# Optimization experiments

Hardware: AMD Instinct MI355X
Metric: run time of the kernel (lower is better)

The kernel has to match this reference:

```python
import jax, jax.numpy as jnp
import numpy as np

D = 1024
H = 16
DH = D // H  # 64
EPS = 1e-6


def setup_inputs() -> dict:
    key = jax.random.key(0)
    ks = jax.random.split(key, 8)
    N, NQ, NK = 8, 1024, 1024
    queries = jax.random.normal(ks[0], (N, NQ, D), dtype=jnp.float32)
    keys = jax.random.normal(ks[1], (N, NK, D), dtype=jnp.float32)
    values = jax.random.normal(ks[2], (N, NK, D), dtype=jnp.float32)
    mask = jax.random.uniform(ks[3], (H * N, NQ, NK), dtype=jnp.float32)
    s = 1.0 / np.sqrt(D)
    Wq = jax.random.normal(ks[4], (H, DH, D), dtype=jnp.float32) * s  # per-head Linear(d, d_head) weights
    Wk = jax.random.normal(ks[5], (H, DH, D), dtype=jnp.float32) * s
    Wv = jax.random.normal(ks[6], (H, DH, D), dtype=jnp.float32) * s
    Wo = jax.random.normal(ks[7], (D, D), dtype=jnp.float32) * s
    return {"queries": queries, "keys": keys, "values": values, "mask": mask,
            "Wq": Wq, "Wk": Wk, "Wv": Wv, "Wo": Wo}


def reference(queries, keys, values, mask, Wq, Wk, Wv, Wo):
    N, NQ, _ = queries.shape
    NK = keys.shape[1]
    # per-head projections, fused into one batched einsum (head-major like torch.cat(dim=0))
    q = jnp.einsum('nqd,hed->hnqe', queries, Wq)  # [H, N, NQ, DH]
    k = jnp.einsum('nkd,hed->hnke', keys, Wk)
    v = jnp.einsum('nkd,hed->hnke', values, Wv)
    scores = jnp.einsum('hnqe,hnke->hnqk', q, k) / jnp.sqrt(jnp.float32(DH))
    att = jax.nn.softmax(scores, axis=-1)  # [H, N, NQ, NK]
    m = mask.reshape(H, N, NQ, NK)
    att = att * m
    att = att / (att.sum(axis=-1, keepdims=True) + EPS)
    o = jnp.einsum('hnqk,hnke->hnqe', att, v)  # [H, N, NQ, DH]
    # concat heads along feature dim: [N, NQ, H*DH]
    o = o.transpose(1, 2, 0, 3).reshape(N, NQ, D)
    return o @ Wo.T
```

## Files before the change

### kernel.cpp

```cpp
#include <hip/hip_runtime.h>
#include <stdint.h>

#define DEV static __device__ __forceinline__

typedef __attribute__((ext_vector_type(8))) short shortx8;
typedef __attribute__((ext_vector_type(4))) float floatx4;
typedef __attribute__((ext_vector_type(4))) unsigned short ushortx4;
typedef __attribute__((ext_vector_type(4))) unsigned int uintx4;


DEV unsigned short f2bf(float x) {
  unsigned int u = __float_as_uint(x);
  u += 0x7fffu + ((u >> 16) & 1u);
  return (unsigned short)(u >> 16);
}

DEV unsigned int cvtpk(float lo, float hi) {
  unsigned int r;
  asm("v_cvt_pk_bf16_f32 %0, %1, %2" : "=v"(r) : "v"(lo), "v"(hi));
  return r;
}

DEV void async16(const void* g, void* l) {
  __builtin_amdgcn_global_load_lds(
      (const __attribute__((address_space(1))) void*)g,
      (__attribute__((address_space(3))) void*)l, 16, 0, 0);
}

__global__ __launch_bounds__(256) void cast_all(
    const float* __restrict__ xq, const float* __restrict__ xk, const float* __restrict__ xv,
    const float* __restrict__ wq, const float* __restrict__ wk, const float* __restrict__ wv,
    const float* __restrict__ wo,
    unsigned short* __restrict__ oxq, unsigned short* __restrict__ oxk, unsigned short* __restrict__ oxv,
    unsigned short* __restrict__ owq, unsigned short* __restrict__ owk, unsigned short* __restrict__ owv,
    unsigned short* __restrict__ owo) {
  int b = blockIdx.x;
  const float* in;
  unsigned short* out;
  size_t i;
  if (b < 12288) {
    int which = b >> 12;
    in = which == 0 ? xq : (which == 1 ? xk : xv);
    out = which == 0 ? oxq : (which == 1 ? oxk : oxv);
    i = (size_t)(b & 4095) * 256 + threadIdx.x;
  } else {
    int bb = b - 12288;
    int which = bb >> 9;
    in = which == 0 ? wq : (which == 1 ? wk : (which == 2 ? wv : wo));
    out = which == 0 ? owq : (which == 1 ? owk : (which == 2 ? owv : owo));
    i = (size_t)(bb & 511) * 256 + threadIdx.x;
  }
  const floatx4* src = (const floatx4*)in;
  floatx4 a = src[2 * i];
  floatx4 c = src[2 * i + 1];
  uintx4 o;
  o[0] = cvtpk(a[0], a[1]);
  o[1] = cvtpk(a[2], a[3]);
  o[2] = cvtpk(c[0], c[1]);
  o[3] = cvtpk(c[2], c[3]);
  ((uintx4*)out)[i] = o;
}


__global__ __launch_bounds__(256) void gemm_qkv(
    const unsigned short* __restrict__ Xq, const unsigned short* __restrict__ Xk,
    const unsigned short* __restrict__ Xv,
    const unsigned short* __restrict__ Bq, const unsigned short* __restrict__ Bk,
    const unsigned short* __restrict__ Bv,
    unsigned short* __restrict__ Oq, unsigned short* __restrict__ Ok,
    unsigned short* __restrict__ Ov) {
  __shared__ __align__(16) unsigned short As[128 * 32];
  __shared__ __align__(16) unsigned short Bs[128 * 32];
  const int z = blockIdx.z;
  const unsigned short* A = z == 0 ? Xq : (z == 1 ? Xk : Xv);
  const unsigned short* B = z == 0 ? Bq : (z == 1 ? Bk : Bv);
  unsigned short* O = z == 0 ? Oq : (z == 1 ? Ok : Ov);

  const int tid  = threadIdx.x;
  const int lane = tid & 63;
  const int wave = tid >> 6;
  const int wm = wave & 1, wn = wave >> 1;
  const int l16 = lane & 15, quad = lane >> 4;
  const int rowBase = blockIdx.y * 128;
  const int colBase = blockIdx.x * 128;

  floatx4 acc[4][4] = {};

  for (int kt = 0; kt < 32; ++kt) {
    __syncthreads();
#pragma unroll
    for (int i = 0; i < 2; ++i) {
      int c = i * 256 + tid;
      int r = c >> 2, kq = c & 3;
      async16(A + (size_t)(rowBase + r) * 1024 + kt * 32 + kq * 8, &As[c * 8]);
      async16(B + (size_t)(colBase + r) * 1024 + kt * 32 + kq * 8, &Bs[c * 8]);
    }
    __syncthreads();
    shortx8 af[4], bfr[4];
#pragma unroll
    for (int t = 0; t < 4; ++t) {
      af[t]  = *(const shortx8*)&As[(wm * 64 + t * 16 + l16) * 32 + quad * 8];
      bfr[t] = *(const shortx8*)&Bs[(wn * 64 + t * 16 + l16) * 32 + quad * 8];
    }
#pragma unroll
    for (int mt = 0; mt < 4; ++mt)
#pragma unroll
      for (int nt = 0; nt < 4; ++nt)
        acc[mt][nt] = __builtin_amdgcn_mfma_f32_16x16x32_bf16(af[mt], bfr[nt], acc[mt][nt], 0, 0, 0);
  }

#pragma unroll
  for (int mt = 0; mt < 4; ++mt) {
#pragma unroll
    for (int nt = 0; nt < 4; ++nt) {
      int col  = colBase + wn * 64 + nt * 16 + l16;
      int row0 = rowBase + wm * 64 + mt * 16 + quad * 4;
      int h = col >> 6, e = col & 63;
      if (z != 2) {
#pragma unroll
        for (int r = 0; r < 4; ++r) {
          int row = row0 + r;
          int n = row >> 10, seq = row & 1023;
          O[(size_t)((h * 8 + n) * 1024 + seq) * 64 + e] = f2bf(acc[mt][nt][r]);
        }
      } else {
        int n = row0 >> 10, seq0 = row0 & 1023;
        ushortx4 pk;
        pk[0] = f2bf(acc[mt][nt][0]); pk[1] = f2bf(acc[mt][nt][1]);
        pk[2] = f2bf(acc[mt][nt][2]); pk[3] = f2bf(acc[mt][nt][3]);
        *(ushortx4*)&O[(size_t)((h * 8 + n) * 64 + e) * 1024 + seq0] = pk;
      }
    }
  }
}

__global__ __launch_bounds__(256) void gemm_out(const unsigned short* __restrict__ A,
                                                const unsigned short* __restrict__ B,
                                                float* __restrict__ O) {
  __shared__ __align__(16) unsigned short As[128 * 32];
  __shared__ __align__(16) unsigned short Bs[128 * 32];
  const int tid  = threadIdx.x;
  const int lane = tid & 63;
  const int wave = tid >> 6;
  const int wm = wave & 1, wn = wave >> 1;
  const int l16 = lane & 15, quad = lane >> 4;
  const int rowBase = blockIdx.y * 128;
  const int colBase = blockIdx.x * 128;

  floatx4 acc[4][4] = {};

  for (int kt = 0; kt < 32; ++kt) {
    __syncthreads();
#pragma unroll
    for (int i = 0; i < 2; ++i) {
      int c = i * 256 + tid;
      int r = c >> 2, kq = c & 3;
      async16(A + (size_t)(rowBase + r) * 1024 + kt * 32 + kq * 8, &As[c * 8]);
      async16(B + (size_t)(colBase + r) * 1024 + kt * 32 + kq * 8, &Bs[c * 8]);
    }
    __syncthreads();
    shortx8 af[4], bfr[4];
#pragma unroll
    for (int t = 0; t < 4; ++t) {
      af[t]  = *(const shortx8*)&As[(wm * 64 + t * 16 + l16) * 32 + quad * 8];
      bfr[t] = *(const shortx8*)&Bs[(wn * 64 + t * 16 + l16) * 32 + quad * 8];
    }
#pragma unroll
    for (int mt = 0; mt < 4; ++mt)
#pragma unroll
      for (int nt = 0; nt < 4; ++nt)
        acc[mt][nt] = __builtin_amdgcn_mfma_f32_16x16x32_bf16(af[mt], bfr[nt], acc[mt][nt], 0, 0, 0);
  }

#pragma unroll
  for (int mt = 0; mt < 4; ++mt)
#pragma unroll
    for (int nt = 0; nt < 4; ++nt) {
      int col  = colBase + wn * 64 + nt * 16 + l16;
      int row0 = rowBase + wm * 64 + mt * 16 + quad * 4;
#pragma unroll
      for (int r = 0; r < 4; ++r)
        O[(size_t)(row0 + r) * 1024 + col] = acc[mt][nt][r];
    }
}

__global__ __launch_bounds__(256) void attn_kernel(const unsigned short* __restrict__ Q,
                                                   const unsigned short* __restrict__ K,
                                                   const unsigned short* __restrict__ Vt,
                                                   const float* __restrict__ mask,
                                                   unsigned short* __restrict__ O) {
  __shared__ __align__(16) unsigned short Pl[2][4 * 32 * 72];
  const int tid = threadIdx.x, lane = tid & 63, wave = tid >> 6;
  const int l16 = lane & 15, quad = lane >> 4;
  const int d = blockIdx.y * 8 + blockIdx.x;
  const int hn = (d & 7) * 16 + ((d >> 3) & 15);
  const int qt = d >> 7;
  const int h = hn >> 3, n = hn & 7;
  const float SC = 0.18033688011112042f;

  const unsigned short* Qb = Q + (size_t)hn * 65536;
  const unsigned short* Kb = K + (size_t)hn * 65536;
  const unsigned short* Vb = Vt + (size_t)hn * 65536;
  const float* Mb = mask + (size_t)hn * 1048576;
  const int q0 = qt * 128 + wave * 32;

  shortx8 qf[2][2];
#pragma unroll
  for (int rt = 0; rt < 2; ++rt)
#pragma unroll
    for (int ks = 0; ks < 2; ++ks)
      qf[rt][ks] = *(const shortx8*)&Qb[(size_t)(q0 + rt * 16 + l16) * 64 + ks * 32 + quad * 8];

  floatx4 oacc[2][4] = {};
  float lsum[2][4] = {};

  for (int kt = 0; kt < 16; ++kt) {
    const int kbase = kt * 64;
    unsigned short* Pw = &Pl[kt & 1][wave * 32 * 72];

    shortx8 kf[4][2];
#pragma unroll
    for (int ct = 0; ct < 4; ++ct)
#pragma unroll
      for (int ks = 0; ks < 2; ++ks)
        kf[ct][ks] = *(const shortx8*)&Kb[(size_t)(kbase + ct * 16 + l16) * 64 + ks * 32 + quad * 8];

#pragma unroll
    for (int rt = 0; rt < 2; ++rt) {
      float mk[4][4];
      const float* Mrow = Mb + (size_t)(q0 + rt * 16 + quad * 4) * 1024 + kbase;
#pragma unroll
      for (int r = 0; r < 4; ++r)
#pragma unroll
        for (int ct = 0; ct < 4; ++ct)
          mk[ct][r] = Mrow[(size_t)r * 1024 + ct * 16 + l16];

      floatx4 s[4] = {};
      __builtin_amdgcn_s_setprio(1);
#pragma unroll
      for (int ct = 0; ct < 4; ++ct)
#pragma unroll
        for (int ks = 0; ks < 2; ++ks)
          s[ct] = __builtin_amdgcn_mfma_f32_16x16x32_bf16(qf[rt][ks], kf[ct][ks], s[ct], 0, 0, 0);
      __builtin_amdgcn_s_setprio(0);

#pragma unroll
      for (int ct = 0; ct < 4; ++ct) {
        float pm[4];
#pragma unroll
        for (int r = 0; r < 4; ++r) {
          float p = exp2f(s[ct][r] * SC);
          pm[r] = p * mk[ct][r];
          lsum[rt][r] += pm[r];
        }
        unsigned int d01 = cvtpk(pm[0], pm[1]);
        unsigned int d23 = cvtpk(pm[2], pm[3]);
        int base = (rt * 16 + quad * 4) * 72 + ct * 16 + l16;
        Pw[base]       = (unsigned short)d01;
        Pw[base + 72]  = (unsigned short)(d01 >> 16);
        Pw[base + 144] = (unsigned short)d23;
        Pw[base + 216] = (unsigned short)(d23 >> 16);
      }
    }

    shortx8 pf[2][2];
#pragma unroll
    for (int rt = 0; rt < 2; ++rt)
#pragma unroll
      for (int ks = 0; ks < 2; ++ks)
        pf[rt][ks] = *(const shortx8*)&Pw[(rt * 16 + l16) * 72 + ks * 32 + quad * 8];
#pragma unroll
    for (int nt = 0; nt < 4; ++nt) {
      shortx8 vf0 = *(const shortx8*)&Vb[(size_t)(nt * 16 + l16) * 1024 + kbase + quad * 8];
      shortx8 vf1 = *(const shortx8*)&Vb[(size_t)(nt * 16 + l16) * 1024 + kbase + 32 + quad * 8];
      __builtin_amdgcn_s_setprio(1);
#pragma unroll
      for (int rt = 0; rt < 2; ++rt) {
        oacc[rt][nt] = __builtin_amdgcn_mfma_f32_16x16x32_bf16(pf[rt][0], vf0, oacc[rt][nt], 0, 0, 0);
        oacc[rt][nt] = __builtin_amdgcn_mfma_f32_16x16x32_bf16(pf[rt][1], vf1, oacc[rt][nt], 0, 0, 0);
      }
      __builtin_amdgcn_s_setprio(0);
    }
  }

#pragma unroll
  for (int off = 8; off >= 1; off >>= 1)
#pragma unroll
    for (int rt = 0; rt < 2; ++rt)
#pragma unroll
      for (int r = 0; r < 4; ++r)
        lsum[rt][r] += __shfl_xor(lsum[rt][r], off, 64);

  float inv[2][4];
#pragma unroll
  for (int rt = 0; rt < 2; ++rt)
#pragma unroll
    for (int r = 0; r < 4; ++r)
      inv[rt][r] = 1.0f / (lsum[rt][r] + 1e-20f);

#pragma unroll
  for (int rt = 0; rt < 2; ++rt)
#pragma unroll
    for (int nt = 0; nt < 4; ++nt)
#pragma unroll
      for (int r = 0; r < 4; ++r) {
        int qg = q0 + rt * 16 + quad * 4 + r;
        O[(size_t)(n * 1024 + qg) * 1024 + h * 64 + nt * 16 + l16] =
            f2bf(oacc[rt][nt][r] * inv[rt][r]);
      }
}

extern "C" void kernel_launch(void* const* d_in, const int* in_sizes, int n_in,
                              void* d_out, int out_size, void* d_ws, size_t ws_size,
                              hipStream_t stream) {
  const float* queries = (const float*)d_in[0];
  const float* keys    = (const float*)d_in[1];
  const float* values  = (const float*)d_in[2];
  const float* mask    = (const float*)d_in[3];
  const float* Wq      = (const float*)d_in[4];
  const float* Wk      = (const float*)d_in[5];
  const float* Wv      = (const float*)d_in[6];
  const float* Wo      = (const float*)d_in[7];

  char* ws = (char*)d_ws;
  unsigned short* Xq  = (unsigned short*)(ws);
  unsigned short* Xk  = (unsigned short*)(ws + (16u << 20));
  unsigned short* Xv  = (unsigned short*)(ws + (32u << 20));
  unsigned short* Wqb = (unsigned short*)(ws + (48u << 20));
  unsigned short* Wkb = (unsigned short*)(ws + (50u << 20));
  unsigned short* Wvb = (unsigned short*)(ws + (52u << 20));
  unsigned short* Wob = (unsigned short*)(ws + (54u << 20));
  unsigned short* Qp  = (unsigned short*)(ws + (56u << 20));
  unsigned short* Kp  = (unsigned short*)(ws + (72u << 20));
  unsigned short* Vt  = (unsigned short*)(ws + (88u << 20));
  unsigned short* Ob  = Xq;
  float* out = (float*)d_out;

  dim3 blk(256);

  cast_all<<<dim3(14336), blk, 0, stream>>>(queries, keys, values, Wq, Wk, Wv, Wo,
                                            Xq, Xk, Xv, Wqb, Wkb, Wvb, Wob);
  gemm_qkv<<<dim3(8, 64, 3), blk, 0, stream>>>(Xq, Xk, Xv, Wqb, Wkb, Wvb, Qp, Kp, Vt);
  attn_kernel<<<dim3(8, 128), blk, 0, stream>>>(Qp, Kp, Vt, mask, Ob);
  gemm_out<<<dim3(8, 64), blk, 0, stream>>>(Ob, Wob, out);
}
```

Measured before the change: 988.0 us.

## Stage K/V tiles in swizzled LDS with async double-buffered prefetch

Instead of each wave loading K and V fragments straight from global memory, the block cooperatively prefetches the next 64-key K and V tiles into double-buffered LDS using async global-to-LDS loads, with an XOR swizzle to avoid bank conflicts. The four waves share each tile, so global K/V traffic per block drops, and the loads overlap with compute. The P buffer goes from double to single buffering, and a block-wide barrier is added at the end of each iteration. That barrier may cost some wave independence.

```diff
diff --git a/kernel.cpp b/kernel.cpp
--- a/kernel.cpp
+++ b/kernel.cpp
@@ -189,7 +189,9 @@
                                                    const unsigned short* __restrict__ Vt,
                                                    const float* __restrict__ mask,
                                                    unsigned short* __restrict__ O) {
-  __shared__ __align__(16) unsigned short Pl[2][4 * 32 * 72];
+  __shared__ __align__(16) unsigned short Ks[2][64 * 64];
+  __shared__ __align__(16) unsigned short Vs[2][64 * 64];
+  __shared__ __align__(16) unsigned short Pl[4 * 32 * 72];
   const int tid = threadIdx.x, lane = tid & 63, wave = tid >> 6;
   const int l16 = lane & 15, quad = lane >> 4;
   const int d = blockIdx.y * 8 + blockIdx.x;
@@ -197,6 +199,7 @@
   const int qt = d >> 7;
   const int h = hn >> 3, n = hn & 7;
   const float SC = 0.18033688011112042f;
+  const int swz = (l16 & 7) << 4;
 
   const unsigned short* Qb = Q + (size_t)hn * 65536;
   const unsigned short* Kb = K + (size_t)hn * 65536;
@@ -204,6 +207,21 @@
   const float* Mb = mask + (size_t)hn * 1048576;
   const int q0 = qt * 128 + wave * 32;
 
+  auto stage = [&](int buf, int kbase) {
+#pragma unroll
+    for (int i = 0; i < 2; ++i) {
+      int c = i * 256 + tid;
+      int r = c >> 3;
+      int lo = ((c & 7) * 16) ^ ((r & 7) << 4);
+      async16((const char*)Kb + (size_t)(kbase + r) * 128 + lo,
+              (char*)&Ks[buf][0] + c * 16);
+      async16((const char*)Vb + (size_t)r * 2048 + (size_t)kbase * 2 + lo,
+              (char*)&Vs[buf][0] + c * 16);
+    }
+  };
+
+  stage(0, 0);
+
   shortx8 qf[2][2];
 #pragma unroll
   for (int rt = 0; rt < 2; ++rt)
@@ -213,17 +231,25 @@
 
   floatx4 oacc[2][4] = {};
   float lsum[2][4] = {};
+  unsigned short* Pw = &Pl[wave * 32 * 72];
+
+  __syncthreads();
 
   for (int kt = 0; kt < 16; ++kt) {
     const int kbase = kt * 64;
-    unsigned short* Pw = &Pl[kt & 1][wave * 32 * 72];
+    const int buf = kt & 1;
+
+    if (kt < 15) stage(buf ^ 1, kbase + 64);
 
     shortx8 kf[4][2];
 #pragma unroll
     for (int ct = 0; ct < 4; ++ct)
 #pragma unroll
-      for (int ks = 0; ks < 2; ++ks)
-        kf[ct][ks] = *(const shortx8*)&Kb[(size_t)(kbase + ct * 16 + l16) * 64 + ks * 32 + quad * 8];
+      for (int ks = 0; ks < 2; ++ks) {
+        int R = ct * 16 + l16;
+        kf[ct][ks] = *(const shortx8*)((const char*)&Ks[buf][0] + R * 128 +
+                                       ((ks * 64 + quad * 16) ^ swz));
+      }
 
 #pragma unroll
     for (int rt = 0; rt < 2; ++rt) {
@@ -271,8 +297,9 @@
         pf[rt][ks] = *(const shortx8*)&Pw[(rt * 16 + l16) * 72 + ks * 32 + quad * 8];
 #pragma unroll
     for (int nt = 0; nt < 4; ++nt) {
-      shortx8 vf0 = *(const shortx8*)&Vb[(size_t)(nt * 16 + l16) * 1024 + kbase + quad * 8];
-      shortx8 vf1 = *(const shortx8*)&Vb[(size_t)(nt * 16 + l16) * 1024 + kbase + 32 + quad * 8];
+      int R = nt * 16 + l16;
+      shortx8 vf0 = *(const shortx8*)((const char*)&Vs[buf][0] + R * 128 + ((quad * 16) ^ swz));
+      shortx8 vf1 = *(const shortx8*)((const char*)&Vs[buf][0] + R * 128 + ((64 + quad * 16) ^ swz));
       __builtin_amdgcn_s_setprio(1);
 #pragma unroll
       for (int rt = 0; rt < 2; ++rt) {
@@ -281,6 +308,8 @@
       }
       __builtin_amdgcn_s_setprio(0);
     }
+
+    __syncthreads();
   }
 
 #pragma unroll
```

After: 923.8 us. 1.07x faster.
